# Performance work log

Measured on AMD Instinct MI355X. Metric: run time of the kernel, lower is better.

## Reference

```python
import jax, jax.numpy as jnp
import numpy as np

B, C, T = 8, 256, 2048
REDUCED = max(C // 8, 8)  # 32


def setup_inputs() -> dict:
    key = jax.random.key(0)
    ks = jax.random.split(key, 7)
    s = 1.0 / np.sqrt(C)
    return {
        "x": jax.random.normal(ks[0], (B, C, T), dtype=jnp.float32),
        "Wq": jax.random.uniform(ks[1], (REDUCED, C), jnp.float32, -s, s),
        "bq": jax.random.uniform(ks[2], (REDUCED,), jnp.float32, -s, s),
        "Wk": jax.random.uniform(ks[3], (REDUCED, C), jnp.float32, -s, s),
        "bk": jax.random.uniform(ks[4], (REDUCED,), jnp.float32, -s, s),
        "Wv": jax.random.uniform(ks[5], (C, C), jnp.float32, -s, s),
        "bv": jax.random.uniform(ks[6], (C,), jnp.float32, -s, s),
        "gamma": jnp.zeros((1,), dtype=jnp.float32) + 0.1,  # nonzero so output depends on attention
    }


def reference(x, Wq, bq, Wk, bk, Wv, bv, gamma):
    # conv1x1 projections == per-timestep linear over channels
    q = jnp.einsum("rc,bct->btr", Wq, x) + bq            # [B, T, reduced]
    k = jnp.einsum("rc,bct->brt", Wk, x) + bk[:, None]   # [B, reduced, T]
    v = jnp.einsum("oc,bct->bto", Wv, x) + bv            # [B, T, C]
    attn = jnp.einsum("btr,brs->bts", q, k)              # [B, T, T]
    attn = jax.nn.softmax(attn, axis=-1)
    out = jnp.einsum("bts,bsc->btc", attn, v)            # [B, T, C]
    out = jnp.transpose(out, (0, 2, 1))                  # [B, C, T]
    return x + gamma * out
```

## Files before the change

kernel.cpp:

```cpp
#include <hip/hip_runtime.h>
#include <hip/hip_bf16.h>
#include <math.h>

constexpr int BB = 8;
constexpr int CC = 256;
constexpr int TT = 2048;
constexpr int RR = 32;

constexpr int VS = 72;
constexpr int PS = 72;
constexpr int OSTR = 68;

constexpr int PT  = 32;
constexpr int XS32 = 33;
constexpr int XSB  = 264;

constexpr float FIXEDM = 24.0f;

typedef short short8 __attribute__((ext_vector_type(8)));
typedef float f32x4 __attribute__((ext_vector_type(4)));
typedef unsigned short us4 __attribute__((ext_vector_type(4)));

static __device__ __forceinline__ unsigned short f2bf(float f) {
    __hip_bfloat16 h = __float2bfloat16(f);
    return *reinterpret_cast<unsigned short*>(&h);
}

__global__ __launch_bounds__(256, 2) void proj_kernel(
    const float* __restrict__ x,
    const float* __restrict__ Wq, const float* __restrict__ bq,
    const float* __restrict__ Wk, const float* __restrict__ bk,
    const float* __restrict__ Wv, const float* __restrict__ bv,
    unsigned short* __restrict__ qws, unsigned short* __restrict__ kws,
    unsigned short* __restrict__ vws)
{
    __shared__ float xs32[CC * XS32];
    __shared__ unsigned short xsb[PT * XSB];

    const int tid = threadIdx.x;
    const int t0  = blockIdx.x * PT;
    const int b   = blockIdx.y;
    const float* xb = x + (size_t)b * CC * TT;

    #pragma unroll
    for (int m = 0; m < 8; ++m) {
        int lin = m * 256 + tid;
        int c   = lin >> 3;
        int t4  = lin & 7;
        float4 v = *(const float4*)(xb + (size_t)c * TT + t0 + t4 * 4);
        float* d = &xs32[c * XS32 + t4 * 4];
        d[0] = v.x; d[1] = v.y; d[2] = v.z; d[3] = v.w;
    }
    __syncthreads();
    {
        int c = tid;
        #pragma unroll
        for (int t = 0; t < PT; ++t)
            xsb[t * XSB + c] = f2bf(xs32[c * XS32 + t]);
    }
    __syncthreads();

    const int lane = tid & 63;
    const int w    = __builtin_amdgcn_readfirstlane(tid >> 6);
    const int l15  = lane & 15;
    const int quad = lane >> 4;

    const float* Wt[5]; const float* bt[5]; int rl[5]; int seg[5];
    #pragma unroll
    for (int i = 0; i < 5; ++i) {
        int mt = w * 5 + i;
        if (mt < 2)      { Wt[i] = Wq; bt[i] = bq; rl[i] = mt * 16;       seg[i] = 0; }
        else if (mt < 4) { Wt[i] = Wk; bt[i] = bk; rl[i] = (mt - 2) * 16; seg[i] = 1; }
        else             { Wt[i] = Wv; bt[i] = bv; rl[i] = (mt - 4) * 16; seg[i] = 2; }
    }

    f32x4 acc[5][2];
    #pragma unroll
    for (int i = 0; i < 5; ++i) {
        float4 bb = *(const float4*)(bt[i] + rl[i] + quad * 4);
        #pragma unroll
        for (int nt = 0; nt < 2; ++nt)
            acc[i][nt] = (f32x4){bb.x, bb.y, bb.z, bb.w};
    }

    #pragma unroll
    for (int ks = 0; ks < 8; ++ks) {
        short8 bfr[2];
        #pragma unroll
        for (int nt = 0; nt < 2; ++nt)
            bfr[nt] = *(const short8*)(&xsb[(nt * 16 + l15) * XSB + ks * 32 + quad * 8]);
        #pragma unroll
        for (int i = 0; i < 5; ++i) {
            const float* wp = Wt[i] + (size_t)(rl[i] + l15) * CC + ks * 32 + quad * 8;
            float4 a0 = *(const float4*)wp;
            float4 a1 = *(const float4*)(wp + 4);
            short8 af;
            af[0] = (short)f2bf(a0.x); af[1] = (short)f2bf(a0.y);
            af[2] = (short)f2bf(a0.z); af[3] = (short)f2bf(a0.w);
            af[4] = (short)f2bf(a1.x); af[5] = (short)f2bf(a1.y);
            af[6] = (short)f2bf(a1.z); af[7] = (short)f2bf(a1.w);
            #pragma unroll
            for (int nt = 0; nt < 2; ++nt)
                acc[i][nt] = __builtin_amdgcn_mfma_f32_16x16x32_bf16(
                    af, bfr[nt], acc[i][nt], 0, 0, 0);
        }
    }

    #pragma unroll
    for (int i = 0; i < 5; ++i) {
        if (seg[i] < 2) {
            unsigned short* outt = (seg[i] == 0 ? qws : kws) + (size_t)b * TT * RR;
            #pragma unroll
            for (int nt = 0; nt < 2; ++nt) {
                int t = t0 + nt * 16 + l15;
                us4 pk;
                pk[0] = f2bf(acc[i][nt][0]); pk[1] = f2bf(acc[i][nt][1]);
                pk[2] = f2bf(acc[i][nt][2]); pk[3] = f2bf(acc[i][nt][3]);
                *(us4*)(outt + (size_t)t * RR + rl[i] + quad * 4) = pk;
            }
        } else {
            unsigned short* vt = vws + (size_t)b * CC * TT;
            #pragma unroll
            for (int nt = 0; nt < 2; ++nt)
                #pragma unroll
                for (int r = 0; r < 4; ++r)
                    vt[(size_t)(rl[i] + quad * 4 + r) * TT + t0 + nt * 16 + l15] =
                        f2bf(acc[i][nt][r]);
        }
    }
}

__global__ __launch_bounds__(512, 2) void attn_kernel(
    const float* __restrict__ x,
    const unsigned short* __restrict__ qws, const unsigned short* __restrict__ kws,
    const unsigned short* __restrict__ vws, const float* __restrict__ gamma_p,
    float* __restrict__ out)
{
    __shared__ __align__(16) unsigned short smem[2 * CC * VS + 2 * 64 * PS];
    __shared__ float lsum[64];
    __shared__ float linv_s[64];

    const int tid  = threadIdx.x;
    const int b    = blockIdx.x;
    const int t0   = blockIdx.y * 64;
    const int lane = tid & 63;
    const int w    = __builtin_amdgcn_readfirstlane(tid >> 6);
    const int g    = w >> 2;
    const int w0   = w & 3;
    const int l15  = lane & 15;
    const int quad = lane >> 4;
    const int tl   = tid & 255;

    unsigned short* Vs = smem + g * (CC * VS);
    unsigned short* Ps = smem + 2 * (CC * VS) + g * (64 * PS);

    const unsigned short* qb = qws + (size_t)b * TT * RR;
    const unsigned short* kb = kws + (size_t)b * TT * RR;
    const unsigned short* vb = vws + (size_t)b * CC * TT;

    short8 qfrag = *(const short8*)(qb + (size_t)(t0 + w0 * 16 + l15) * RR + quad * 8);

    float rs[4];
    #pragma unroll
    for (int r = 0; r < 4; ++r) rs[r] = 0.0f;

    f32x4 acc[4][4];
    #pragma unroll
    for (int mt = 0; mt < 4; ++mt)
        #pragma unroll
        for (int nt = 0; nt < 4; ++nt)
            acc[mt][nt] = (f32x4){0.f, 0.f, 0.f, 0.f};

    const f32x4 zz = (f32x4){0.f, 0.f, 0.f, 0.f};

    short8 vreg[8], kreg[4];
    {
        int s0 = g * 64;
        #pragma unroll
        for (int m = 0; m < 8; ++m) {
            int lin = m * 256 + tl;
            int c   = lin >> 3;
            int s8  = lin & 7;
            vreg[m] = *(const short8*)(vb + (size_t)c * TT + s0 + s8 * 8);
        }
        #pragma unroll
        for (int nt = 0; nt < 4; ++nt)
            kreg[nt] = *(const short8*)(kb + (size_t)(s0 + nt * 16 + l15) * RR + quad * 8);
    }

    for (int j = 0; j < 16; ++j) {
        __syncthreads();

        #pragma unroll
        for (int m = 0; m < 8; ++m) {
            int lin = m * 256 + tl;
            int c   = lin >> 3;
            int s8  = lin & 7;
            *(short8*)(&Vs[c * VS + s8 * 8]) = vreg[m];
        }

        f32x4 st[4];
        #pragma unroll
        for (int nt = 0; nt < 4; ++nt)
            st[nt] = __builtin_amdgcn_mfma_f32_16x16x32_bf16(qfrag, kreg[nt], zz, 0, 0, 0);

        const int prow = w0 * 16 + quad * 4;
        #pragma unroll
        for (int nt = 0; nt < 4; ++nt) {
            #pragma unroll
            for (int r = 0; r < 4; ++r) {
                float e = __expf(st[nt][r] - FIXEDM);
                rs[r] += e;
                Ps[(prow + r) * PS + nt * 16 + l15] = f2bf(e);
            }
        }
        __syncthreads();

        if (j < 15) {
            int s1 = (j + 1) * 128 + g * 64;
            #pragma unroll
            for (int m = 0; m < 8; ++m) {
                int lin = m * 256 + tl;
                int c   = lin >> 3;
                int s8  = lin & 7;
                vreg[m] = *(const short8*)(vb + (size_t)c * TT + s1 + s8 * 8);
            }
            #pragma unroll
            for (int nt = 0; nt < 4; ++nt)
                kreg[nt] = *(const short8*)(kb + (size_t)(s1 + nt * 16 + l15) * RR + quad * 8);
        }

        #pragma unroll
        for (int ks = 0; ks < 2; ++ks) {
            short8 pa[4], vf[4];
            #pragma unroll
            for (int mt = 0; mt < 4; ++mt)
                pa[mt] = *(const short8*)(&Ps[(mt * 16 + l15) * PS + ks * 32 + quad * 8]);
            #pragma unroll
            for (int nt = 0; nt < 4; ++nt)
                vf[nt] = *(const short8*)(&Vs[(w0 * 64 + nt * 16 + l15) * VS + ks * 32 + quad * 8]);
            #pragma unroll
            for (int mt = 0; mt < 4; ++mt)
                #pragma unroll
                for (int nt = 0; nt < 4; ++nt)
                    acc[mt][nt] = __builtin_amdgcn_mfma_f32_16x16x32_bf16(
                        pa[mt], vf[nt], acc[mt][nt], 0, 0, 0);
        }
    }

    #pragma unroll
    for (int mask = 1; mask < 16; mask <<= 1)
        #pragma unroll
        for (int r = 0; r < 4; ++r)
            rs[r] += __shfl_xor(rs[r], mask, 64);

    __syncthreads();

    float* scratch = (float*)smem;
    if (g == 1) {
        #pragma unroll
        for (int mt = 0; mt < 4; ++mt)
            #pragma unroll
            for (int nt = 0; nt < 4; ++nt)
                *(f32x4*)(&scratch[(w0 * 64 + nt * 16 + l15) * OSTR + mt * 16 + quad * 4]) =
                    acc[mt][nt];
        if (l15 == 0) {
            #pragma unroll
            for (int r = 0; r < 4; ++r) lsum[w0 * 16 + quad * 4 + r] = rs[r];
        }
    }
    __syncthreads();

    if (g == 0) {
        #pragma unroll
        for (int mt = 0; mt < 4; ++mt)
            #pragma unroll
            for (int nt = 0; nt < 4; ++nt) {
                f32x4 o = *(const f32x4*)(&scratch[(w0 * 64 + nt * 16 + l15) * OSTR + mt * 16 + quad * 4]);
                acc[mt][nt][0] += o[0]; acc[mt][nt][1] += o[1];
                acc[mt][nt][2] += o[2]; acc[mt][nt][3] += o[3];
            }
        #pragma unroll
        for (int r = 0; r < 4; ++r) rs[r] += lsum[w0 * 16 + quad * 4 + r];
        if (l15 == 0) {
            #pragma unroll
            for (int r = 0; r < 4; ++r)
                linv_s[w0 * 16 + quad * 4 + r] = 1.0f / rs[r];
        }

        const float gam = gamma_p[0];
        const float* xb = x + (size_t)b * CC * TT;
        float* ob = out + (size_t)b * CC * TT;

        #pragma unroll
        for (int mt = 0; mt < 4; ++mt) {
            f32x4 li4 = *(const f32x4*)(&linv_s[mt * 16 + quad * 4]);
            #pragma unroll
            for (int nt = 0; nt < 4; ++nt) {
                int c = w0 * 64 + nt * 16 + l15;
                size_t gidx = (size_t)c * TT + t0 + mt * 16 + quad * 4;
                float4 xv = *(const float4*)(xb + gidx);
                float4 ov;
                ov.x = xv.x + gam * acc[mt][nt][0] * li4[0];
                ov.y = xv.y + gam * acc[mt][nt][1] * li4[1];
                ov.z = xv.z + gam * acc[mt][nt][2] * li4[2];
                ov.w = xv.w + gam * acc[mt][nt][3] * li4[3];
                *(float4*)(ob + gidx) = ov;
            }
        }
    }
}

extern "C" void kernel_launch(void* const* d_in, const int* in_sizes, int n_in,
                              void* d_out, int out_size, void* d_ws, size_t ws_size,
                              hipStream_t stream)
{
    const float* x     = (const float*)d_in[0];
    const float* Wq    = (const float*)d_in[1];
    const float* bq    = (const float*)d_in[2];
    const float* Wk    = (const float*)d_in[3];
    const float* bk    = (const float*)d_in[4];
    const float* Wv    = (const float*)d_in[5];
    const float* bv    = (const float*)d_in[6];
    const float* gamma = (const float*)d_in[7];
    float* out = (float*)d_out;

    unsigned short* qws = (unsigned short*)d_ws;
    unsigned short* kws = qws + (size_t)BB * TT * RR;
    unsigned short* vws = kws + (size_t)BB * TT * RR;

    dim3 pgrid(TT / PT, BB);
    proj_kernel<<<pgrid, 256, 0, stream>>>(x, Wq, bq, Wk, bk, Wv, bv, qws, kws, vws);

    dim3 agrid(BB, TT / 64);
    attn_kernel<<<agrid, 512, 0, stream>>>(x, qws, kws, vws, gamma, out);
}
```

Baseline: 149.6 us.

## Load V fragments directly from global into registers and pre-cast weights to bf16

```diff
diff --git a/kernel.cpp b/kernel.cpp
--- a/kernel.cpp
+++ b/kernel.cpp
@@ -7,7 +7,6 @@
 constexpr int TT = 2048;
 constexpr int RR = 32;
 
-constexpr int VS = 72;
 constexpr int PS = 72;
 constexpr int OSTR = 68;
 
@@ -26,11 +25,28 @@
     return *reinterpret_cast<unsigned short*>(&h);
 }
 
+__global__ __launch_bounds__(256) void wcast_kernel(
+    const float* __restrict__ Wq, const float* __restrict__ Wk,
+    const float* __restrict__ Wv,
+    unsigned short* __restrict__ wqb, unsigned short* __restrict__ wkb,
+    unsigned short* __restrict__ wvb)
+{
+    int g = blockIdx.x * 256 + threadIdx.x;
+    const float* src; unsigned short* dst; int i4;
+    if (g < 2048)       { src = Wq; dst = wqb; i4 = g; }
+    else if (g < 4096)  { src = Wk; dst = wkb; i4 = g - 2048; }
+    else                { src = Wv; dst = wvb; i4 = g - 4096; }
+    float4 v = *(const float4*)(src + i4 * 4);
+    us4 p;
+    p[0] = f2bf(v.x); p[1] = f2bf(v.y); p[2] = f2bf(v.z); p[3] = f2bf(v.w);
+    *(us4*)(dst + i4 * 4) = p;
+}
+
 __global__ __launch_bounds__(256, 2) void proj_kernel(
     const float* __restrict__ x,
-    const float* __restrict__ Wq, const float* __restrict__ bq,
-    const float* __restrict__ Wk, const float* __restrict__ bk,
-    const float* __restrict__ Wv, const float* __restrict__ bv,
+    const unsigned short* __restrict__ wqb, const float* __restrict__ bq,
+    const unsigned short* __restrict__ wkb, const float* __restrict__ bk,
+    const unsigned short* __restrict__ wvb, const float* __restrict__ bv,
     unsigned short* __restrict__ qws, unsigned short* __restrict__ kws,
     unsigned short* __restrict__ vws)
 {
@@ -65,13 +81,13 @@
     const int l15  = lane & 15;
     const int quad = lane >> 4;
 
-    const float* Wt[5]; const float* bt[5]; int rl[5]; int seg[5];
+    const unsigned short* Wt[5]; const float* bt[5]; int rl[5]; int seg[5];
     #pragma unroll
     for (int i = 0; i < 5; ++i) {
         int mt = w * 5 + i;
-        if (mt < 2)      { Wt[i] = Wq; bt[i] = bq; rl[i] = mt * 16;       seg[i] = 0; }
-        else if (mt < 4) { Wt[i] = Wk; bt[i] = bk; rl[i] = (mt - 2) * 16; seg[i] = 1; }
-        else             { Wt[i] = Wv; bt[i] = bv; rl[i] = (mt - 4) * 16; seg[i] = 2; }
+        if (mt < 2)      { Wt[i] = wqb; bt[i] = bq; rl[i] = mt * 16;       seg[i] = 0; }
+        else if (mt < 4) { Wt[i] = wkb; bt[i] = bk; rl[i] = (mt - 2) * 16; seg[i] = 1; }
+        else             { Wt[i] = wvb; bt[i] = bv; rl[i] = (mt - 4) * 16; seg[i] = 2; }
     }
 
     f32x4 acc[5][2];
@@ -91,14 +107,7 @@
             bfr[nt] = *(const short8*)(&xsb[(nt * 16 + l15) * XSB + ks * 32 + quad * 8]);
         #pragma unroll
         for (int i = 0; i < 5; ++i) {
-            const float* wp = Wt[i] + (size_t)(rl[i] + l15) * CC + ks * 32 + quad * 8;
-            float4 a0 = *(const float4*)wp;
-            float4 a1 = *(const float4*)(wp + 4);
-            short8 af;
-            af[0] = (short)f2bf(a0.x); af[1] = (short)f2bf(a0.y);
-            af[2] = (short)f2bf(a0.z); af[3] = (short)f2bf(a0.w);
-            af[4] = (short)f2bf(a1.x); af[5] = (short)f2bf(a1.y);
-            af[6] = (short)f2bf(a1.z); af[7] = (short)f2bf(a1.w);
+            short8 af = *(const short8*)(Wt[i] + (size_t)(rl[i] + l15) * CC + ks * 32 + quad * 8);
             #pragma unroll
             for (int nt = 0; nt < 2; ++nt)
                 acc[i][nt] = __builtin_amdgcn_mfma_f32_16x16x32_bf16(
@@ -136,7 +145,7 @@
     const unsigned short* __restrict__ vws, const float* __restrict__ gamma_p,
     float* __restrict__ out)
 {
-    __shared__ __align__(16) unsigned short smem[2 * CC * VS + 2 * 64 * PS];
+    __shared__ __align__(16) char smem[CC * OSTR * 4];
     __shared__ float lsum[64];
     __shared__ float linv_s[64];
 
@@ -149,10 +158,8 @@
     const int w0   = w & 3;
     const int l15  = lane & 15;
     const int quad = lane >> 4;
-    const int tl   = tid & 255;
-
-    unsigned short* Vs = smem + g * (CC * VS);
-    unsigned short* Ps = smem + 2 * (CC * VS) + g * (64 * PS);
+
+    unsigned short* Ps = (unsigned short*)smem + g * (64 * PS);
 
     const unsigned short* qb = qws + (size_t)b * TT * RR;
     const unsigned short* kb = kws + (size_t)b * TT * RR;
@@ -173,36 +180,34 @@
 
     const f32x4 zz = (f32x4){0.f, 0.f, 0.f, 0.f};
 
-    short8 vreg[8], kreg[4];
+    const unsigned short* vbase = vb + (size_t)(w0 * 64 + l15) * TT + quad * 8;
+
+    short8 kcur[4], vcur[8];
     {
         int s0 = g * 64;
         #pragma unroll
-        for (int m = 0; m < 8; ++m) {
-            int lin = m * 256 + tl;
-            int c   = lin >> 3;
-            int s8  = lin & 7;
-            vreg[m] = *(const short8*)(vb + (size_t)c * TT + s0 + s8 * 8);
-        }
-        #pragma unroll
         for (int nt = 0; nt < 4; ++nt)
-            kreg[nt] = *(const short8*)(kb + (size_t)(s0 + nt * 16 + l15) * RR + quad * 8);
+            kcur[nt] = *(const short8*)(kb + (size_t)(s0 + nt * 16 + l15) * RR + quad * 8);
+        #pragma unroll
+        for (int ks = 0; ks < 2; ++ks)
+            #pragma unroll
+            for (int nt = 0; nt < 4; ++nt)
+                vcur[ks * 4 + nt] = *(const short8*)(vbase + (size_t)(nt * 16) * TT + s0 + ks * 32);
     }
 
     for (int j = 0; j < 16; ++j) {
-        __syncthreads();
-
-        #pragma unroll
-        for (int m = 0; m < 8; ++m) {
-            int lin = m * 256 + tl;
-            int c   = lin >> 3;
-            int s8  = lin & 7;
-            *(short8*)(&Vs[c * VS + s8 * 8]) = vreg[m];
-        }
-
         f32x4 st[4];
         #pragma unroll
         for (int nt = 0; nt < 4; ++nt)
-            st[nt] = __builtin_amdgcn_mfma_f32_16x16x32_bf16(qfrag, kreg[nt], zz, 0, 0, 0);
+            st[nt] = __builtin_amdgcn_mfma_f32_16x16x32_bf16(qfrag, kcur[nt], zz, 0, 0, 0);
+
+        short8 knext[4];
+        if (j < 15) {
+            int s1 = (j + 1) * 128 + g * 64;
+            #pragma unroll
+            for (int nt = 0; nt < 4; ++nt)
+                knext[nt] = *(const short8*)(kb + (size_t)(s1 + nt * 16 + l15) * RR + quad * 8);
+        }
 
         const int prow = w0 * 16 + quad * 4;
         #pragma unroll
@@ -216,36 +221,35 @@
         }
         __syncthreads();
 
+        short8 vnext[8];
         if (j < 15) {
             int s1 = (j + 1) * 128 + g * 64;
             #pragma unroll
-            for (int m = 0; m < 8; ++m) {
-                int lin = m * 256 + tl;
-                int c   = lin >> 3;
-                int s8  = lin & 7;
-                vreg[m] = *(const short8*)(vb + (size_t)c * TT + s1 + s8 * 8);
-            }
-            #pragma unroll
-            for (int nt = 0; nt < 4; ++nt)
-                kreg[nt] = *(const short8*)(kb + (size_t)(s1 + nt * 16 + l15) * RR + quad * 8);
+            for (int ks = 0; ks < 2; ++ks)
+                #pragma unroll
+                for (int nt = 0; nt < 4; ++nt)
+                    vnext[ks * 4 + nt] = *(const short8*)(vbase + (size_t)(nt * 16) * TT + s1 + ks * 32);
         }
 
         #pragma unroll
         for (int ks = 0; ks < 2; ++ks) {
-            short8 pa[4], vf[4];
+            short8 pa[4];
             #pragma unroll
             for (int mt = 0; mt < 4; ++mt)
                 pa[mt] = *(const short8*)(&Ps[(mt * 16 + l15) * PS + ks * 32 + quad * 8]);
-            #pragma unroll
-            for (int nt = 0; nt < 4; ++nt)
-                vf[nt] = *(const short8*)(&Vs[(w0 * 64 + nt * 16 + l15) * VS + ks * 32 + quad * 8]);
             #pragma unroll
             for (int mt = 0; mt < 4; ++mt)
                 #pragma unroll
                 for (int nt = 0; nt < 4; ++nt)
                     acc[mt][nt] = __builtin_amdgcn_mfma_f32_16x16x32_bf16(
-                        pa[mt], vf[nt], acc[mt][nt], 0, 0, 0);
-        }
+                        pa[mt], vcur[ks * 4 + nt], acc[mt][nt], 0, 0, 0);
+        }
+        __syncthreads();
+
+        #pragma unroll
+        for (int nt = 0; nt < 4; ++nt) kcur[nt] = knext[nt];
+        #pragma unroll
+        for (int m = 0; m < 8; ++m) vcur[m] = vnext[m];
     }
 
     #pragma unroll
@@ -328,9 +332,14 @@
     unsigned short* qws = (unsigned short*)d_ws;
     unsigned short* kws = qws + (size_t)BB * TT * RR;
     unsigned short* vws = kws + (size_t)BB * TT * RR;
+    unsigned short* wqb = vws + (size_t)BB * CC * TT;
+    unsigned short* wkb = wqb + (size_t)RR * CC;
+    unsigned short* wvb = wkb + (size_t)RR * CC;
+
+    wcast_kernel<<<80, 256, 0, stream>>>(Wq, Wk, Wv, wqb, wkb, wvb);
 
     dim3 pgrid(TT / PT, BB);
-    proj_kernel<<<pgrid, 256, 0, stream>>>(x, Wq, bq, Wk, bk, Wv, bv, qws, kws, vws);
+    proj_kernel<<<pgrid, 256, 0, stream>>>(x, wqb, bq, wkb, bk, wvb, bv, qws, kws, vws);
 
     dim3 agrid(BB, TT / 64);
     attn_kernel<<<agrid, 512, 0, stream>>>(x, qws, kws, vws, gamma, out);
```

Measured after the change: 147.7 us. Within noise of the previous version (-1.3%).
